# Performance work log

Hardware: AMD Instinct MI355X
Metric: run time of the kernel (lower is better)

The kernel has to match this reference:

```python
import jax, jax.numpy as jnp
import numpy as np

ALPHA = 0.2        # LeakyReLU negative slope
NEG_BIG = -9e15    # mask fill value from the original module


def setup_inputs() -> dict:
    key = jax.random.key(0)
    k1, k2, k3, k4 = jax.random.split(key, 4)
    B, N, F_in, F_out = 4, 4096, 128, 64
    h = jax.random.normal(k1, (B, N, F_in), dtype=jnp.float32)
    adj = jax.random.randint(k2, (N, N), 0, 2, dtype=jnp.int32)
    W = jax.random.normal(k3, (F_in, F_out), dtype=jnp.float32)
    a = jax.random.normal(k4, (2 * F_out, 1), dtype=jnp.float32)
    return {"h": h, "adj": adj, "W": W, "a": a}


def reference(h, adj, W, a):
    # h: [B, N, F_in], adj: [N, N], W: [F_in, F_out], a: [2*F_out, 1]
    F_out = W.shape[1]
    hW = jnp.einsum('bni,io->bno', h, W)               # [B, N, F_out]
    f1 = hW @ a[:F_out, :]                             # [B, N, 1]
    f2 = hW @ a[F_out:, :]                             # [B, N, 1]
    e = f1 + jnp.swapaxes(f2, 1, 2)                    # [B, N, N] broadcast-add
    e = jax.nn.leaky_relu(e, negative_slope=ALPHA)
    e = jax.nn.softmax(e, axis=2)
    # dropout is a no-op (is_training=False)
    attention = jnp.where(adj[None, :, :] > 0, e, NEG_BIG)
    new_h = jax.nn.sigmoid(jnp.einsum('bnm,bmo->bno', attention, hW))
    return new_h
```

## Files before the change

kernel.cpp:

```cpp
#include <hip/hip_runtime.h>
#include <hip/hip_bf16.h>


#define GN 4096
#define GB 4
#define FIN 128
#define FOUT 64

typedef int i32x4 __attribute__((ext_vector_type(4)));
typedef unsigned int uint32x4 __attribute__((ext_vector_type(4)));
typedef float f32x4 __attribute__((ext_vector_type(4)));
typedef float f32x2 __attribute__((ext_vector_type(2)));

__global__ __launch_bounds__(256) void front_kernel(const int* __restrict__ adj,
                                                    const float* __restrict__ h,
                                                    const float* __restrict__ W,
                                                    unsigned long long* __restrict__ tmask,
                                                    double* __restrict__ hW,
                                                    unsigned char* __restrict__ Bp) {
    __shared__ unsigned short m16[64][68];
    __shared__ double hsd[4][FIN];
    __shared__ unsigned int dg[4][64];

    if (blockIdx.x < 256) {
        const int t = threadIdx.x;
        const int rt = (int)blockIdx.x >> 2, cp = (int)blockIdx.x & 3;
        const int row = t >> 2, jq = t & 3;
        const int* rbase = adj + (size_t)(rt * 64 + row) * GN + cp * 1024;
#pragma unroll
        for (int it = 0; it < 16; ++it) {
            const int j16 = it * 4 + jq;
            const i32x4* p = (const i32x4*)(rbase + j16 * 16);
            unsigned int b16 = 0;
#pragma unroll
            for (int q = 0; q < 4; ++q) {
                i32x4 v = p[q];
                b16 |= (v.x == 0 ? 1u : 0u) << (q * 4);
                b16 |= (v.y == 0 ? 2u : 0u) << (q * 4);
                b16 |= (v.z == 0 ? 4u : 0u) << (q * 4);
                b16 |= (v.w == 0 ? 8u : 0u) << (q * 4);
            }
            m16[row][j16] = (unsigned short)b16;
        }
        __syncthreads();
#pragma unroll
        for (int it = 0; it < 4; ++it) {
            const int idx = it * 256 + t;
            const int sloc = idx >> 6, l = idx & 63;
            const int row16 = l & 15, g = l >> 4;
            unsigned long long res = 0ull;
#pragma unroll
            for (int r = 0; r < 4; ++r)
                res |= (unsigned long long)m16[r * 16 + row16][sloc * 4 + g] << (r * 16);
            tmask[((size_t)rt * 64 + cp * 16 + sloc) * 64 + l] = res;
        }
    } else {
        const int bx = (int)blockIdx.x - 256;
        const int grp = threadIdx.x >> 6;
        const int o = threadIdx.x & 63;
        const int b = bx >> 10, q4 = bx & 1023;
        {
            const f32x2* src = (const f32x2*)(h + ((size_t)b * GN + q4 * 4) * FIN);
            f32x2 v = src[threadIdx.x];
            double* drow = &hsd[threadIdx.x >> 6][(threadIdx.x & 63) * 2];
            drow[0] = (double)v.x;
            drow[1] = (double)v.y;
        }
        __syncthreads();
        double a0 = 0, a1 = 0, a2 = 0, a3 = 0;
#pragma unroll
        for (int i = 0; i < FIN; i += 4) {
            a0 = fma(hsd[grp][i],     (double)W[i * FOUT + o],       a0);
            a1 = fma(hsd[grp][i + 1], (double)W[(i + 1) * FOUT + o], a1);
            a2 = fma(hsd[grp][i + 2], (double)W[(i + 2) * FOUT + o], a2);
            a3 = fma(hsd[grp][i + 3], (double)W[(i + 3) * FOUT + o], a3);
        }
        double acc = (a0 + a1) + (a2 + a3);
        hW[((size_t)b * GN + q4 * 4 + grp) * FOUT + o] = acc;

        int qi = (int)llrint(acc * 65536.0);
        int d0 = ((qi + 128) & 255) - 128; qi = (qi - d0) >> 8;
        int d1 = ((qi + 128) & 255) - 128; qi = (qi - d1) >> 8;
        dg[grp][o] = (unsigned int)(d0 & 255) | ((unsigned int)(d1 & 255) << 8)
                   | ((unsigned int)(qi & 255) << 16);
        __syncthreads();
        if (grp < 3) {
            unsigned int w = 0;
#pragma unroll
            for (int rr = 0; rr < 4; ++rr)
                w |= ((dg[rr][o] >> (grp * 8)) & 255u) << (rr * 8);
            const int p = q4 >> 4, g = (q4 >> 2) & 3, qr = q4 & 3;
            const int cg = o >> 4, col16 = o & 15;
            *(unsigned int*)(Bp + ((size_t)b * 64 + p) * 12288 + grp * 4096
                             + cg * 1024 + g * 256 + col16 * 16 + qr * 4) = w;
        }
    }
}

__global__ __launch_bounds__(512, 1) void gemm_kernel(const unsigned char* __restrict__ Bp,
                                                      const unsigned long long* __restrict__ tmask,
                                                      const double* __restrict__ hW,
                                                      float* __restrict__ out) {
    __shared__ __align__(16) unsigned char lds[49152];
    __shared__ unsigned int nflag;
    __shared__ unsigned int flagbuf[128];
    __shared__ double fred[8];

    const int tid = threadIdx.x, lane = tid & 63, wv = tid >> 6;
    const int cg = wv & 3, kg = wv >> 2;
    const int rt = (int)blockIdx.x >> 2, b = (int)blockIdx.x & 3;
    if (tid == 0) nflag = 0;

    const unsigned char* bptr = Bp + (size_t)b * 786432 + kg * 12288 + cg * 1024 + lane * 16;
    const unsigned long long* mptr = tmask + (size_t)rt * 4096 + kg * 64 + lane;

    i32x4 acc[4][3];
#pragma unroll
    for (int r = 0; r < 4; ++r)
#pragma unroll
        for (int pl = 0; pl < 3; ++pl) {
            i32x4 z = {0, 0, 0, 0};
            acc[r][pl] = z;
        }

#define DECLSET(S) i32x4 b##S##0, b##S##1, b##S##2; unsigned long long m##S;
#define LOADSET(S, T) { const unsigned char* g_ = bptr + (size_t)(T) * 24576;          \
        b##S##0 = *(const i32x4*)(g_);                                                 \
        b##S##1 = *(const i32x4*)(g_ + 4096);                                          \
        b##S##2 = *(const i32x4*)(g_ + 8192);                                          \
        m##S = mptr[(size_t)(T) * 128]; }

    DECLSET(A) DECLSET(B) DECLSET(C) DECLSET(D)
    LOADSET(A, 0) LOADSET(B, 1) LOADSET(C, 2) LOADSET(D, 3)

    auto dostep = [&](unsigned long long mw, i32x4 v0, i32x4 v1, i32x4 v2) {
        const unsigned int mlo = (unsigned int)mw, mhi = (unsigned int)(mw >> 32);
#pragma unroll
        for (int r = 0; r < 4; ++r) {
            unsigned int half = (r >> 1) ? mhi : mlo;
            unsigned int w16 = (r & 1) ? (half >> 16) : (half & 0xFFFFu);
            uint32x4 u;
#pragma unroll
            for (int q = 0; q < 4; ++q)
                u[q] = (((w16 >> (4 * q)) & 0xFu) * 0x00204081u) & 0x01010101u;
            i32x4 af = __builtin_bit_cast(i32x4, u);
            acc[r][0] = __builtin_amdgcn_mfma_i32_16x16x64_i8(af, v0, acc[r][0], 0, 0, 0);
            acc[r][1] = __builtin_amdgcn_mfma_i32_16x16x64_i8(af, v1, acc[r][1], 0, 0, 0);
            acc[r][2] = __builtin_amdgcn_mfma_i32_16x16x64_i8(af, v2, acc[r][2], 0, 0, 0);
        }
    };

    for (int T = 0; T < 32; T += 4) {
        dostep(mA, bA0, bA1, bA2);
        if (T + 4 < 32) LOADSET(A, T + 4)
        dostep(mB, bB0, bB1, bB2);
        if (T + 5 < 32) LOADSET(B, T + 5)
        dostep(mC, bC0, bC1, bC2);
        if (T + 6 < 32) LOADSET(C, T + 6)
        dostep(mD, bD0, bD1, bD2);
        if (T + 7 < 32) LOADSET(D, T + 7)
    }
#undef DECLSET
#undef LOADSET

    __syncthreads();
    if (kg == 1) {
        unsigned char* dst = lds + cg * 12288 + lane * 192;
#pragma unroll
        for (int r = 0; r < 4; ++r)
#pragma unroll
            for (int pl = 0; pl < 3; ++pl)
                *(i32x4*)(dst + (r * 3 + pl) * 16) = acc[r][pl];
    }
    __syncthreads();
    if (kg == 0) {
        const unsigned char* s2 = lds + cg * 12288 + lane * 192;
#pragma unroll
        for (int r = 0; r < 4; ++r)
#pragma unroll
            for (int pl = 0; pl < 3; ++pl) {
                i32x4 v = *(const i32x4*)(s2 + (r * 3 + pl) * 16);
#pragma unroll
                for (int q = 0; q < 4; ++q) acc[r][pl][q] += v[q];
            }

        const int o = cg * 16 + (lane & 15);
#pragma unroll
        for (int r = 0; r < 4; ++r) {
#pragma unroll
            for (int q = 0; q < 4; ++q) {
                double S = (double)acc[r][0][q] + 256.0 * (double)acc[r][1][q]
                         + 65536.0 * (double)acc[r][2][q];
                int i = rt * 64 + r * 16 + (lane >> 4) * 4 + q;
                size_t oi = ((size_t)b * GN + i) * FOUT + o;
                out[oi] = S < 0.0 ? 1.0f : 0.0f;
                if (fabs(S) <= 2048.0) {
                    unsigned int idx = atomicAdd(&nflag, 1u);
                    if (idx < 128) flagbuf[idx] = ((unsigned int)i << 6) | (unsigned int)o;
                }
            }
        }
    }

    __syncthreads();
    unsigned int nf = nflag;
    if (nf > 128) nf = 128;
    for (unsigned int f = 0; f < nf; ++f) {
        unsigned int e = flagbuf[f];
        int o = e & 63;
        int i = (int)(e >> 6);
        int row16 = i & 15, r = (i >> 4) & 3;
        int s = tid >> 3, lg = (tid >> 1) & 3, hf = tid & 1;
        unsigned long long w = tmask[((size_t)rt * 64 + s) * 64 + (lg * 16 + row16)];
        double ps = 0.0;
        const double* hwc = hW + ((size_t)b * GN + s * 64 + lg * 16) * FOUT + o;
#pragma unroll
        for (int jj = hf * 8; jj < hf * 8 + 8; ++jj) {
            if ((w >> (r * 16 + jj)) & 1ull)
                ps += hwc[(size_t)jj * FOUT];
        }
#pragma unroll
        for (int d = 32; d >= 1; d >>= 1) ps += __shfl_down(ps, d, 64);
        if (lane == 0) fred[wv] = ps;
        __syncthreads();
        if (tid == 0) {
            double tot = ((fred[0] + fred[1]) + (fred[2] + fred[3]))
                       + ((fred[4] + fred[5]) + (fred[6] + fred[7]));
            out[((size_t)b * GN + i) * FOUT + o] = tot < 0.0 ? 1.0f : 0.0f;
        }
        __syncthreads();
    }
}

extern "C" void kernel_launch(void* const* d_in, const int* in_sizes, int n_in,
                              void* d_out, int out_size, void* d_ws, size_t ws_size,
                              hipStream_t stream) {
    const float* h   = (const float*)d_in[0];
    const int*   adj = (const int*)d_in[1];
    const float* W   = (const float*)d_in[2];
    float* out = (float*)d_out;

    char* ws = (char*)d_ws;
    double* hW                = (double*)ws;
    unsigned char* Bp         = (unsigned char*)(ws + 8388608);
    unsigned long long* tmask = (unsigned long long*)(ws + 12582912);

    front_kernel<<<4352, 256, 0, stream>>>(adj, h, W, tmask, hW, Bp);
    gemm_kernel<<<256, 512, 0, stream>>>(Bp, tmask, hW, out);
}
```

Measured before the change: 57.51 us.

## Split front kernel into adjacency pack and hW repack kernels, stage W in LDS

The fused front kernel is split into two launches. A pack kernel builds each 64-bit transposed mask word directly from global memory, with no LDS staging or block sync. A hW kernel first converts all of W to double in LDS, so the dot-product loop reads shared memory instead of global memory. In exchange there is one extra kernel launch, every block reloads the whole 64 KB W, and the 64 KB LDS per block limits occupancy.

```diff
diff --git a/kernel.cpp b/kernel.cpp
--- a/kernel.cpp
+++ b/kernel.cpp
@@ -12,88 +12,83 @@
 typedef float f32x4 __attribute__((ext_vector_type(4)));
 typedef float f32x2 __attribute__((ext_vector_type(2)));
 
-__global__ __launch_bounds__(256) void front_kernel(const int* __restrict__ adj,
-                                                    const float* __restrict__ h,
-                                                    const float* __restrict__ W,
-                                                    unsigned long long* __restrict__ tmask,
-                                                    double* __restrict__ hW,
-                                                    unsigned char* __restrict__ Bp) {
-    __shared__ unsigned short m16[64][68];
+__global__ __launch_bounds__(256) void pack_kernel(const int* __restrict__ adj,
+                                                   unsigned long long* __restrict__ tmask) {
+    int wid = blockIdx.x * 4 + (threadIdx.x >> 6);
+    int lane = threadIdx.x & 63;
+    int rt = wid >> 6, s = wid & 63;
+    int row16 = lane & 15, g = lane >> 4;
+    const int* base = adj + (size_t)(rt * 64 + row16) * GN + s * 64 + g * 16;
+    unsigned long long res = 0ull;
+#pragma unroll
+    for (int r = 0; r < 4; ++r) {
+        const i32x4* p = (const i32x4*)(base + (size_t)r * 16 * GN);
+        unsigned int b16 = 0;
+#pragma unroll
+        for (int q = 0; q < 4; ++q) {
+            i32x4 v = p[q];
+            b16 |= (v.x == 0 ? 1u : 0u) << (q * 4);
+            b16 |= (v.y == 0 ? 2u : 0u) << (q * 4);
+            b16 |= (v.z == 0 ? 4u : 0u) << (q * 4);
+            b16 |= (v.w == 0 ? 8u : 0u) << (q * 4);
+        }
+        res |= (unsigned long long)b16 << (r * 16);
+    }
+    tmask[(size_t)wid * 64 + lane] = res;
+}
+
+__global__ __launch_bounds__(256, 1) void hwrepack_kernel(const float* __restrict__ h,
+                                                          const float* __restrict__ W,
+                                                          double* __restrict__ hW,
+                                                          unsigned char* __restrict__ Bp) {
+    __shared__ double Wd[FIN][FOUT];
     __shared__ double hsd[4][FIN];
     __shared__ unsigned int dg[4][64];
 
-    if (blockIdx.x < 256) {
-        const int t = threadIdx.x;
-        const int rt = (int)blockIdx.x >> 2, cp = (int)blockIdx.x & 3;
-        const int row = t >> 2, jq = t & 3;
-        const int* rbase = adj + (size_t)(rt * 64 + row) * GN + cp * 1024;
-#pragma unroll
-        for (int it = 0; it < 16; ++it) {
-            const int j16 = it * 4 + jq;
-            const i32x4* p = (const i32x4*)(rbase + j16 * 16);
-            unsigned int b16 = 0;
-#pragma unroll
-            for (int q = 0; q < 4; ++q) {
-                i32x4 v = p[q];
-                b16 |= (v.x == 0 ? 1u : 0u) << (q * 4);
-                b16 |= (v.y == 0 ? 2u : 0u) << (q * 4);
-                b16 |= (v.z == 0 ? 4u : 0u) << (q * 4);
-                b16 |= (v.w == 0 ? 8u : 0u) << (q * 4);
-            }
-            m16[row][j16] = (unsigned short)b16;
-        }
-        __syncthreads();
-#pragma unroll
-        for (int it = 0; it < 4; ++it) {
-            const int idx = it * 256 + t;
-            const int sloc = idx >> 6, l = idx & 63;
-            const int row16 = l & 15, g = l >> 4;
-            unsigned long long res = 0ull;
-#pragma unroll
-            for (int r = 0; r < 4; ++r)
-                res |= (unsigned long long)m16[r * 16 + row16][sloc * 4 + g] << (r * 16);
-            tmask[((size_t)rt * 64 + cp * 16 + sloc) * 64 + l] = res;
-        }
-    } else {
-        const int bx = (int)blockIdx.x - 256;
-        const int grp = threadIdx.x >> 6;
-        const int o = threadIdx.x & 63;
-        const int b = bx >> 10, q4 = bx & 1023;
-        {
-            const f32x2* src = (const f32x2*)(h + ((size_t)b * GN + q4 * 4) * FIN);
-            f32x2 v = src[threadIdx.x];
-            double* drow = &hsd[threadIdx.x >> 6][(threadIdx.x & 63) * 2];
-            drow[0] = (double)v.x;
-            drow[1] = (double)v.y;
-        }
-        __syncthreads();
-        double a0 = 0, a1 = 0, a2 = 0, a3 = 0;
-#pragma unroll
-        for (int i = 0; i < FIN; i += 4) {
-            a0 = fma(hsd[grp][i],     (double)W[i * FOUT + o],       a0);
-            a1 = fma(hsd[grp][i + 1], (double)W[(i + 1) * FOUT + o], a1);
-            a2 = fma(hsd[grp][i + 2], (double)W[(i + 2) * FOUT + o], a2);
-            a3 = fma(hsd[grp][i + 3], (double)W[(i + 3) * FOUT + o], a3);
-        }
-        double acc = (a0 + a1) + (a2 + a3);
-        hW[((size_t)b * GN + q4 * 4 + grp) * FOUT + o] = acc;
-
-        int qi = (int)llrint(acc * 65536.0);
-        int d0 = ((qi + 128) & 255) - 128; qi = (qi - d0) >> 8;
-        int d1 = ((qi + 128) & 255) - 128; qi = (qi - d1) >> 8;
-        dg[grp][o] = (unsigned int)(d0 & 255) | ((unsigned int)(d1 & 255) << 8)
-                   | ((unsigned int)(qi & 255) << 16);
-        __syncthreads();
-        if (grp < 3) {
-            unsigned int w = 0;
-#pragma unroll
-            for (int rr = 0; rr < 4; ++rr)
-                w |= ((dg[rr][o] >> (grp * 8)) & 255u) << (rr * 8);
-            const int p = q4 >> 4, g = (q4 >> 2) & 3, qr = q4 & 3;
-            const int cg = o >> 4, col16 = o & 15;
-            *(unsigned int*)(Bp + ((size_t)b * 64 + p) * 12288 + grp * 4096
-                             + cg * 1024 + g * 256 + col16 * 16 + qr * 4) = w;
-        }
+    const int grp = threadIdx.x >> 6;
+    const int o = threadIdx.x & 63;
+    const int b = (int)blockIdx.x >> 10, q4 = (int)blockIdx.x & 1023;
+
+#pragma unroll
+    for (int c = 0; c < 32; ++c) {
+        int idx = c * 256 + threadIdx.x;
+        Wd[idx >> 6][idx & 63] = (double)W[idx];
+    }
+    {
+        const f32x2* src = (const f32x2*)(h + ((size_t)b * GN + q4 * 4) * FIN);
+        f32x2 v = src[threadIdx.x];
+        double* drow = &hsd[threadIdx.x >> 6][(threadIdx.x & 63) * 2];
+        drow[0] = (double)v.x;
+        drow[1] = (double)v.y;
+    }
+    __syncthreads();
+
+    double a0 = 0, a1 = 0, a2 = 0, a3 = 0;
+#pragma unroll
+    for (int i = 0; i < FIN; i += 4) {
+        a0 = fma(hsd[grp][i],     Wd[i][o],     a0);
+        a1 = fma(hsd[grp][i + 1], Wd[i + 1][o], a1);
+        a2 = fma(hsd[grp][i + 2], Wd[i + 2][o], a2);
+        a3 = fma(hsd[grp][i + 3], Wd[i + 3][o], a3);
+    }
+    double acc = (a0 + a1) + (a2 + a3);
+    hW[((size_t)b * GN + q4 * 4 + grp) * FOUT + o] = acc;
+
+    int qi = (int)llrint(acc * 65536.0);
+    int d0 = ((qi + 128) & 255) - 128; qi = (qi - d0) >> 8;
+    int d1 = ((qi + 128) & 255) - 128; qi = (qi - d1) >> 8;
+    dg[grp][o] = (unsigned int)(d0 & 255) | ((unsigned int)(d1 & 255) << 8)
+               | ((unsigned int)(qi & 255) << 16);
+    __syncthreads();
+    if (grp < 3) {
+        unsigned int w = 0;
+#pragma unroll
+        for (int rr = 0; rr < 4; ++rr)
+            w |= ((dg[rr][o] >> (grp * 8)) & 255u) << (rr * 8);
+        const int p = q4 >> 4, g = (q4 >> 2) & 3, qr = q4 & 3;
+        const int cg = o >> 4, col16 = o & 15;
+        *(unsigned int*)(Bp + ((size_t)b * 64 + p) * 12288 + grp * 4096
+                         + cg * 1024 + g * 256 + col16 * 16 + qr * 4) = w;
     }
 }
 
@@ -245,6 +240,7 @@
     unsigned char* Bp         = (unsigned char*)(ws + 8388608);
     unsigned long long* tmask = (unsigned long long*)(ws + 12582912);
 
-    front_kernel<<<4352, 256, 0, stream>>>(adj, h, W, tmask, hW, Bp);
+    pack_kernel<<<1024, 256, 0, stream>>>(adj, tmask);
+    hwrepack_kernel<<<4096, 256, 0, stream>>>(h, W, hW, Bp);
     gemm_kernel<<<256, 512, 0, stream>>>(Bp, tmask, hW, out);
 }
```

After: 73.43 us. 27.7% more time.

## Fuse front and GEMM kernels into one cooperative kernel with grid sync

Applied to the files above, without the earlier changes.

Merges the mask-packing/hW-projection kernel and the int8 MFMA GEMM kernel into a single cooperative launch of 256 blocks × 512 threads, separated by a grid-wide sync. Each block now packs its adjacency tile and computes 16 hW row-groups in a loop, then runs the GEMM. This removes a kernel launch boundary and its tail, at the cost of fewer blocks doing the front work, serialized per-iteration barriers in the projection loop, and the overhead of a grid barrier.

```diff
diff --git a/kernel.cpp b/kernel.cpp
--- a/kernel.cpp
+++ b/kernel.cpp
@@ -1,5 +1,8 @@
 #include <hip/hip_runtime.h>
 #include <hip/hip_bf16.h>
+#include <hip/hip_cooperative_groups.h>
+
+namespace cg = cooperative_groups;
 
 
 #define GN 4096
@@ -10,31 +13,34 @@
 typedef int i32x4 __attribute__((ext_vector_type(4)));
 typedef unsigned int uint32x4 __attribute__((ext_vector_type(4)));
 typedef float f32x4 __attribute__((ext_vector_type(4)));
-typedef float f32x2 __attribute__((ext_vector_type(2)));
-
-__global__ __launch_bounds__(256) void front_kernel(const int* __restrict__ adj,
-                                                    const float* __restrict__ h,
-                                                    const float* __restrict__ W,
-                                                    unsigned long long* __restrict__ tmask,
-                                                    double* __restrict__ hW,
-                                                    unsigned char* __restrict__ Bp) {
-    __shared__ unsigned short m16[64][68];
-    __shared__ double hsd[4][FIN];
-    __shared__ unsigned int dg[4][64];
-
-    if (blockIdx.x < 256) {
-        const int t = threadIdx.x;
-        const int rt = (int)blockIdx.x >> 2, cp = (int)blockIdx.x & 3;
-        const int row = t >> 2, jq = t & 3;
-        const int* rbase = adj + (size_t)(rt * 64 + row) * GN + cp * 1024;
-#pragma unroll
-        for (int it = 0; it < 16; ++it) {
-            const int j16 = it * 4 + jq;
-            const i32x4* p = (const i32x4*)(rbase + j16 * 16);
+
+__global__ __launch_bounds__(512, 1)
+void fused_kernel(const int* __restrict__ adj, const float* __restrict__ h,
+                  const float* __restrict__ W, unsigned long long* __restrict__ tmask,
+                  double* __restrict__ hW, unsigned char* __restrict__ Bp,
+                  float* __restrict__ out) {
+    __shared__ __align__(16) unsigned char SMEM[49152];
+    __shared__ unsigned int nflag;
+    __shared__ unsigned int flagbuf[128];
+    __shared__ double fred[8];
+
+    const int t = threadIdx.x;
+    const int bid = (int)blockIdx.x;
+
+    {
+        unsigned short (*m16)[68] = (unsigned short (*)[68])SMEM;
+        const int rt = bid >> 2, cp = bid & 3;
+        const int wrow = t >> 6;
+        const int j16 = t & 63;
+#pragma unroll
+        for (int p = 0; p < 8; ++p) {
+            const int row = p * 8 + wrow;
+            const i32x4* src = (const i32x4*)(adj + (size_t)(rt * 64 + row) * GN
+                                              + cp * 1024 + j16 * 16);
             unsigned int b16 = 0;
 #pragma unroll
             for (int q = 0; q < 4; ++q) {
-                i32x4 v = p[q];
+                i32x4 v = src[q];
                 b16 |= (v.x == 0 ? 1u : 0u) << (q * 4);
                 b16 |= (v.y == 0 ? 2u : 0u) << (q * 4);
                 b16 |= (v.z == 0 ? 4u : 0u) << (q * 4);
@@ -44,8 +50,8 @@
         }
         __syncthreads();
 #pragma unroll
-        for (int it = 0; it < 4; ++it) {
-            const int idx = it * 256 + t;
+        for (int it = 0; it < 2; ++it) {
+            const int idx = it * 512 + t;
             const int sloc = idx >> 6, l = idx & 63;
             const int row16 = l & 15, g = l >> 4;
             unsigned long long res = 0ull;
@@ -54,74 +60,77 @@
                 res |= (unsigned long long)m16[r * 16 + row16][sloc * 4 + g] << (r * 16);
             tmask[((size_t)rt * 64 + cp * 16 + sloc) * 64 + l] = res;
         }
-    } else {
-        const int bx = (int)blockIdx.x - 256;
-        const int grp = threadIdx.x >> 6;
-        const int o = threadIdx.x & 63;
-        const int b = bx >> 10, q4 = bx & 1023;
-        {
-            const f32x2* src = (const f32x2*)(h + ((size_t)b * GN + q4 * 4) * FIN);
-            f32x2 v = src[threadIdx.x];
-            double* drow = &hsd[threadIdx.x >> 6][(threadIdx.x & 63) * 2];
-            drow[0] = (double)v.x;
-            drow[1] = (double)v.y;
-        }
-        __syncthreads();
-        double a0 = 0, a1 = 0, a2 = 0, a3 = 0;
-#pragma unroll
-        for (int i = 0; i < FIN; i += 4) {
-            a0 = fma(hsd[grp][i],     (double)W[i * FOUT + o],       a0);
-            a1 = fma(hsd[grp][i + 1], (double)W[(i + 1) * FOUT + o], a1);
-            a2 = fma(hsd[grp][i + 2], (double)W[(i + 2) * FOUT + o], a2);
-            a3 = fma(hsd[grp][i + 3], (double)W[(i + 3) * FOUT + o], a3);
-        }
-        double acc = (a0 + a1) + (a2 + a3);
-        hW[((size_t)b * GN + q4 * 4 + grp) * FOUT + o] = acc;
-
-        int qi = (int)llrint(acc * 65536.0);
-        int d0 = ((qi + 128) & 255) - 128; qi = (qi - d0) >> 8;
-        int d1 = ((qi + 128) & 255) - 128; qi = (qi - d1) >> 8;
-        dg[grp][o] = (unsigned int)(d0 & 255) | ((unsigned int)(d1 & 255) << 8)
-                   | ((unsigned int)(qi & 255) << 16);
-        __syncthreads();
-        if (grp < 3) {
-            unsigned int w = 0;
-#pragma unroll
-            for (int rr = 0; rr < 4; ++rr)
-                w |= ((dg[rr][o] >> (grp * 8)) & 255u) << (rr * 8);
-            const int p = q4 >> 4, g = (q4 >> 2) & 3, qr = q4 & 3;
-            const int cg = o >> 4, col16 = o & 15;
-            *(unsigned int*)(Bp + ((size_t)b * 64 + p) * 12288 + grp * 4096
-                             + cg * 1024 + g * 256 + col16 * 16 + qr * 4) = w;
-        }
+        __syncthreads();
     }
-}
-
-__global__ __launch_bounds__(512, 1) void gemm_kernel(const unsigned char* __restrict__ Bp,
-                                                      const unsigned long long* __restrict__ tmask,
-                                                      const double* __restrict__ hW,
-                                                      float* __restrict__ out) {
-    __shared__ __align__(16) unsigned char lds[49152];
-    __shared__ unsigned int nflag;
-    __shared__ unsigned int flagbuf[128];
-    __shared__ double fred[8];
-
-    const int tid = threadIdx.x, lane = tid & 63, wv = tid >> 6;
-    const int cg = wv & 3, kg = wv >> 2;
-    const int rt = (int)blockIdx.x >> 2, b = (int)blockIdx.x & 3;
-    if (tid == 0) nflag = 0;
-
-    const unsigned char* bptr = Bp + (size_t)b * 786432 + kg * 12288 + cg * 1024 + lane * 16;
-    const unsigned long long* mptr = tmask + (size_t)rt * 4096 + kg * 64 + lane;
-
-    i32x4 acc[4][3];
-#pragma unroll
-    for (int r = 0; r < 4; ++r)
-#pragma unroll
-        for (int pl = 0; pl < 3; ++pl) {
-            i32x4 z = {0, 0, 0, 0};
-            acc[r][pl] = z;
-        }
+
+    {
+        float (*hs)[4][FIN] = (float (*)[4][FIN])SMEM;
+        unsigned int (*dg)[4][64] = (unsigned int (*)[4][64])(SMEM + 8192);
+        const int sub = t >> 8;
+        const int tt = t & 255;
+        const int grp = tt >> 6, o = tt & 63;
+
+#pragma unroll
+        for (int u = 0; u < 8; ++u) {
+            const int v = bid * 16 + sub * 8 + u;
+            const int b = v >> 10, q4 = v & 1023;
+            if (tt < 128) {
+                const f32x4* src = (const f32x4*)(h + ((size_t)b * GN + q4 * 4) * FIN);
+                f32x4* dst = (f32x4*)&hs[sub][0][0];
+                dst[tt] = src[tt];
+            }
+            __syncthreads();
+            double a0 = 0, a1 = 0, a2 = 0, a3 = 0;
+#pragma unroll
+            for (int i = 0; i < FIN; i += 4) {
+                a0 = fma((double)hs[sub][grp][i],     (double)W[i * FOUT + o],       a0);
+                a1 = fma((double)hs[sub][grp][i + 1], (double)W[(i + 1) * FOUT + o], a1);
+                a2 = fma((double)hs[sub][grp][i + 2], (double)W[(i + 2) * FOUT + o], a2);
+                a3 = fma((double)hs[sub][grp][i + 3], (double)W[(i + 3) * FOUT + o], a3);
+            }
+            double acc = (a0 + a1) + (a2 + a3);
+            hW[((size_t)b * GN + q4 * 4 + grp) * FOUT + o] = acc;
+
+            int qi = (int)llrint(acc * 65536.0);
+            int d0 = ((qi + 128) & 255) - 128; qi = (qi - d0) >> 8;
+            int d1 = ((qi + 128) & 255) - 128; qi = (qi - d1) >> 8;
+            dg[sub][grp][o] = (unsigned int)(d0 & 255) | ((unsigned int)(d1 & 255) << 8)
+                            | ((unsigned int)(qi & 255) << 16);
+            __syncthreads();
+            if (grp < 3) {
+                unsigned int w = 0;
+#pragma unroll
+                for (int rr = 0; rr < 4; ++rr)
+                    w |= ((dg[sub][rr][o] >> (grp * 8)) & 255u) << (rr * 8);
+                const int p = q4 >> 4, g = (q4 >> 2) & 3, qr = q4 & 3;
+                const int cgi = o >> 4, col16 = o & 15;
+                *(unsigned int*)(Bp + ((size_t)b * 64 + p) * 12288 + grp * 4096
+                                 + cgi * 1024 + g * 256 + col16 * 16 + qr * 4) = w;
+            }
+            __syncthreads();
+        }
+    }
+
+    cg::this_grid().sync();
+
+    {
+        unsigned char* lds = SMEM;
+        const int tid = t, lane = tid & 63, wv = tid >> 6;
+        const int cgr = wv & 3, kg = wv >> 2;
+        const int rt = bid >> 2, b = bid & 3;
+        if (tid == 0) nflag = 0;
+
+        const unsigned char* bptr = Bp + (size_t)b * 786432 + kg * 12288 + cgr * 1024 + lane * 16;
+        const unsigned long long* mptr = tmask + (size_t)rt * 4096 + kg * 64 + lane;
+
+        i32x4 acc[4][3];
+#pragma unroll
+        for (int r = 0; r < 4; ++r)
+#pragma unroll
+            for (int pl = 0; pl < 3; ++pl) {
+                i32x4 z = {0, 0, 0, 0};
+                acc[r][pl] = z;
+            }
 
 #define DECLSET(S) i32x4 b##S##0, b##S##1, b##S##2; unsigned long long m##S;
 #define LOADSET(S, T) { const unsigned char* g_ = bptr + (size_t)(T) * 24576;          \
@@ -130,113 +139,114 @@
         b##S##2 = *(const i32x4*)(g_ + 8192);                                          \
         m##S = mptr[(size_t)(T) * 128]; }
 
-    DECLSET(A) DECLSET(B) DECLSET(C) DECLSET(D)
-    LOADSET(A, 0) LOADSET(B, 1) LOADSET(C, 2) LOADSET(D, 3)
-
-    auto dostep = [&](unsigned long long mw, i32x4 v0, i32x4 v1, i32x4 v2) {
-        const unsigned int mlo = (unsigned int)mw, mhi = (unsigned int)(mw >> 32);
-#pragma unroll
-        for (int r = 0; r < 4; ++r) {
-            unsigned int half = (r >> 1) ? mhi : mlo;
-            unsigned int w16 = (r & 1) ? (half >> 16) : (half & 0xFFFFu);
-            uint32x4 u;
-#pragma unroll
-            for (int q = 0; q < 4; ++q)
-                u[q] = (((w16 >> (4 * q)) & 0xFu) * 0x00204081u) & 0x01010101u;
-            i32x4 af = __builtin_bit_cast(i32x4, u);
-            acc[r][0] = __builtin_amdgcn_mfma_i32_16x16x64_i8(af, v0, acc[r][0], 0, 0, 0);
-            acc[r][1] = __builtin_amdgcn_mfma_i32_16x16x64_i8(af, v1, acc[r][1], 0, 0, 0);
-            acc[r][2] = __builtin_amdgcn_mfma_i32_16x16x64_i8(af, v2, acc[r][2], 0, 0, 0);
-        }
-    };
-
-    for (int T = 0; T < 32; T += 4) {
-        dostep(mA, bA0, bA1, bA2);
-        if (T + 4 < 32) LOADSET(A, T + 4)
-        dostep(mB, bB0, bB1, bB2);
-        if (T + 5 < 32) LOADSET(B, T + 5)
-        dostep(mC, bC0, bC1, bC2);
-        if (T + 6 < 32) LOADSET(C, T + 6)
-        dostep(mD, bD0, bD1, bD2);
-        if (T + 7 < 32) LOADSET(D, T + 7)
-    }
+        DECLSET(A) DECLSET(B) DECLSET(C) DECLSET(D)
+        LOADSET(A, 0) LOADSET(B, 1) LOADSET(C, 2) LOADSET(D, 3)
+
+        auto dostep = [&](unsigned long long mw, i32x4 v0, i32x4 v1, i32x4 v2) {
+            const unsigned int mlo = (unsigned int)mw, mhi = (unsigned int)(mw >> 32);
+#pragma unroll
+            for (int r = 0; r < 4; ++r) {
+                unsigned int half = (r >> 1) ? mhi : mlo;
+                unsigned int w16 = (r & 1) ? (half >> 16) : (half & 0xFFFFu);
+                uint32x4 u;
+#pragma unroll
+                for (int q = 0; q < 4; ++q)
+                    u[q] = (((w16 >> (4 * q)) & 0xFu) * 0x00204081u) & 0x01010101u;
+                i32x4 af = __builtin_bit_cast(i32x4, u);
+                acc[r][0] = __builtin_amdgcn_mfma_i32_16x16x64_i8(af, v0, acc[r][0], 0, 0, 0);
+                acc[r][1] = __builtin_amdgcn_mfma_i32_16x16x64_i8(af, v1, acc[r][1], 0, 0, 0);
+                acc[r][2] = __builtin_amdgcn_mfma_i32_16x16x64_i8(af, v2, acc[r][2], 0, 0, 0);
+            }
+        };
+
+        for (int T = 0; T < 32; T += 4) {
+            dostep(mA, bA0, bA1, bA2);
+            if (T + 4 < 32) LOADSET(A, T + 4)
+            dostep(mB, bB0, bB1, bB2);
+            if (T + 5 < 32) LOADSET(B, T + 5)
+            dostep(mC, bC0, bC1, bC2);
+            if (T + 6 < 32) LOADSET(C, T + 6)
+            dostep(mD, bD0, bD1, bD2);
+            if (T + 7 < 32) LOADSET(D, T + 7)
+        }
 #undef DECLSET
 #undef LOADSET
 
-    __syncthreads();
-    if (kg == 1) {
-        unsigned char* dst = lds + cg * 12288 + lane * 192;
-#pragma unroll
-        for (int r = 0; r < 4; ++r)
-#pragma unroll
-            for (int pl = 0; pl < 3; ++pl)
-                *(i32x4*)(dst + (r * 3 + pl) * 16) = acc[r][pl];
-    }
-    __syncthreads();
-    if (kg == 0) {
-        const unsigned char* s2 = lds + cg * 12288 + lane * 192;
-#pragma unroll
-        for (int r = 0; r < 4; ++r)
-#pragma unroll
-            for (int pl = 0; pl < 3; ++pl) {
-                i32x4 v = *(const i32x4*)(s2 + (r * 3 + pl) * 16);
-#pragma unroll
-                for (int q = 0; q < 4; ++q) acc[r][pl][q] += v[q];
-            }
-
-        const int o = cg * 16 + (lane & 15);
-#pragma unroll
-        for (int r = 0; r < 4; ++r) {
-#pragma unroll
-            for (int q = 0; q < 4; ++q) {
-                double S = (double)acc[r][0][q] + 256.0 * (double)acc[r][1][q]
-                         + 65536.0 * (double)acc[r][2][q];
-                int i = rt * 64 + r * 16 + (lane >> 4) * 4 + q;
-                size_t oi = ((size_t)b * GN + i) * FOUT + o;
-                out[oi] = S < 0.0 ? 1.0f : 0.0f;
-                if (fabs(S) <= 2048.0) {
-                    unsigned int idx = atomicAdd(&nflag, 1u);
-                    if (idx < 128) flagbuf[idx] = ((unsigned int)i << 6) | (unsigned int)o;
+        __syncthreads();
+        if (kg == 1) {
+            unsigned char* dst = lds + cgr * 12288 + lane * 192;
+#pragma unroll
+            for (int r = 0; r < 4; ++r)
+#pragma unroll
+                for (int pl = 0; pl < 3; ++pl)
+                    *(i32x4*)(dst + (r * 3 + pl) * 16) = acc[r][pl];
+        }
+        __syncthreads();
+        if (kg == 0) {
+            const unsigned char* s2 = lds + cgr * 12288 + lane * 192;
+#pragma unroll
+            for (int r = 0; r < 4; ++r)
+#pragma unroll
+                for (int pl = 0; pl < 3; ++pl) {
+                    i32x4 v = *(const i32x4*)(s2 + (r * 3 + pl) * 16);
+#pragma unroll
+                    for (int q = 0; q < 4; ++q) acc[r][pl][q] += v[q];
                 }
-            }
-        }
-    }
-
-    __syncthreads();
-    unsigned int nf = nflag;
-    if (nf > 128) nf = 128;
-    for (unsigned int f = 0; f < nf; ++f) {
-        unsigned int e = flagbuf[f];
-        int o = e & 63;
-        int i = (int)(e >> 6);
-        int row16 = i & 15, r = (i >> 4) & 3;
-        int s = tid >> 3, lg = (tid >> 1) & 3, hf = tid & 1;
-        unsigned long long w = tmask[((size_t)rt * 64 + s) * 64 + (lg * 16 + row16)];
-        double ps = 0.0;
-        const double* hwc = hW + ((size_t)b * GN + s * 64 + lg * 16) * FOUT + o;
-#pragma unroll
-        for (int jj = hf * 8; jj < hf * 8 + 8; ++jj) {
-            if ((w >> (r * 16 + jj)) & 1ull)
-                ps += hwc[(size_t)jj * FOUT];
-        }
-#pragma unroll
-        for (int d = 32; d >= 1; d >>= 1) ps += __shfl_down(ps, d, 64);
-        if (lane == 0) fred[wv] = ps;
-        __syncthreads();
-        if (tid == 0) {
-            double tot = ((fred[0] + fred[1]) + (fred[2] + fred[3]))
-                       + ((fred[4] + fred[5]) + (fred[6] + fred[7]));
-            out[((size_t)b * GN + i) * FOUT + o] = tot < 0.0 ? 1.0f : 0.0f;
-        }
-        __syncthreads();
+
+            const int o = cgr * 16 + (lane & 15);
+#pragma unroll
+            for (int r = 0; r < 4; ++r) {
+#pragma unroll
+                for (int q = 0; q < 4; ++q) {
+                    double S = (double)acc[r][0][q] + 256.0 * (double)acc[r][1][q]
+                             + 65536.0 * (double)acc[r][2][q];
+                    int i = rt * 64 + r * 16 + (lane >> 4) * 4 + q;
+                    size_t oi = ((size_t)b * GN + i) * FOUT + o;
+                    out[oi] = S < 0.0 ? 1.0f : 0.0f;
+                    if (fabs(S) <= 2048.0) {
+                        unsigned int idx = atomicAdd(&nflag, 1u);
+                        if (idx < 128) flagbuf[idx] = ((unsigned int)i << 6) | (unsigned int)o;
+                    }
+                }
+            }
+        }
+
+        __syncthreads();
+        unsigned int nf = nflag;
+        if (nf > 128) nf = 128;
+        for (unsigned int f = 0; f < nf; ++f) {
+            unsigned int e = flagbuf[f];
+            int o = e & 63;
+            int i = (int)(e >> 6);
+            int row16 = i & 15, r = (i >> 4) & 3;
+            int s = tid >> 3, lg = (tid >> 1) & 3, hf = tid & 1;
+            unsigned long long w = tmask[((size_t)rt * 64 + s) * 64 + (lg * 16 + row16)];
+            double ps = 0.0;
+            const double* hwc = hW + ((size_t)b * GN + s * 64 + lg * 16) * FOUT + o;
+#pragma unroll
+            for (int jj = hf * 8; jj < hf * 8 + 8; ++jj) {
+                if ((w >> (r * 16 + jj)) & 1ull)
+                    ps += hwc[(size_t)jj * FOUT];
+            }
+#pragma unroll
+            for (int d = 32; d >= 1; d >>= 1) ps += __shfl_down(ps, d, 64);
+            if (lane == 0) fred[wv] = ps;
+            __syncthreads();
+            if (tid == 0) {
+                double tot = ((fred[0] + fred[1]) + (fred[2] + fred[3]))
+                           + ((fred[4] + fred[5]) + (fred[6] + fred[7]));
+                out[((size_t)b * GN + i) * FOUT + o] = tot < 0.0 ? 1.0f : 0.0f;
+            }
+            __syncthreads();
+        }
     }
 }
 
 extern "C" void kernel_launch(void* const* d_in, const int* in_sizes, int n_in,
                               void* d_out, int out_size, void* d_ws, size_t ws_size,
                               hipStream_t stream) {
+    const int*   adj = (const int*)d_in[1];
     const float* h   = (const float*)d_in[0];
-    const int*   adj = (const int*)d_in[1];
     const float* W   = (const float*)d_in[2];
     float* out = (float*)d_out;
 
@@ -245,6 +255,8 @@
     unsigned char* Bp         = (unsigned char*)(ws + 8388608);
     unsigned long long* tmask = (unsigned long long*)(ws + 12582912);
 
-    front_kernel<<<4352, 256, 0, stream>>>(adj, h, W, tmask, hW, Bp);
-    gemm_kernel<<<256, 512, 0, stream>>>(Bp, tmask, hW, out);
+    void* kargs[] = {(void*)&adj, (void*)&h, (void*)&W,
+                     (void*)&tmask, (void*)&hW, (void*)&Bp, (void*)&out};
+    hipLaunchCooperativeKernel((void*)fused_kernel, dim3(256), dim3(512),
+                               kargs, 0, stream);
 }
```

Result: slower. 172.3 us (+199.6%).
